# Kernel optimization log

Hardware: AMD Instinct MI355X
Metric: run time of the kernel (lower is better)

## Reference

```python
import jax, jax.numpy as jnp
import numpy as np

EPS = 1e-16


def setup_inputs() -> dict:
    key = jax.random.key(0)
    ks = jax.random.split(key, 7)
    B, N, C = 4096, 2048, 128  # batch of heads, memory rows, memory cols
    k = jax.random.normal(ks[0], (B, C), dtype=jnp.float32)
    beta = jax.random.normal(ks[1], (B, 1), dtype=jnp.float32)
    g = jax.random.normal(ks[2], (B, 1), dtype=jnp.float32)
    s = jax.random.normal(ks[3], (B, 3), dtype=jnp.float32)
    gamma = jax.random.normal(ks[4], (B, 1), dtype=jnp.float32)
    w_prev = jax.random.uniform(ks[5], (B, N), dtype=jnp.float32)
    w_prev = w_prev / jnp.sum(w_prev, axis=1, keepdims=True)  # valid weighting
    M = jax.random.normal(ks[6], (N, C), dtype=jnp.float32)  # memory matrix
    return {"k": k, "beta": beta, "g": g, "s": s, "gamma": gamma,
            "w_prev": w_prev, "M": M}


def reference(k, beta, g, s, gamma, w_prev, M):
    # head activations
    beta = jax.nn.softplus(beta)            # [B,1] key strength > 0
    g = jax.nn.sigmoid(g)                   # [B,1] interpolation gate
    s = jax.nn.softmax(s, axis=-1)          # [B,3] shift distribution
    gamma = 1.0 + jax.nn.softplus(gamma)    # [B,1] sharpening >= 1

    # content addressing: cosine similarity k vs memory rows
    k_norm = jnp.linalg.norm(k, axis=-1, keepdims=True)          # [B,1]
    m_norm = jnp.linalg.norm(M, axis=-1, keepdims=True)          # [N,1]
    sim = jnp.einsum('bc,nc->bn', k, M) / (k_norm * m_norm.T + EPS)  # [B,N]
    w_c = jax.nn.softmax(beta * sim, axis=-1)                    # [B,N]

    # interpolation with previous weighting
    w_g = g * w_c + (1.0 - g) * w_prev                           # [B,N]

    # circular convolution with 3-tap shift kernel (shifts -1, 0, +1)
    w_tilde = (s[:, 0:1] * jnp.roll(w_g, 1, axis=1)
               + s[:, 1:2] * w_g
               + s[:, 2:3] * jnp.roll(w_g, -1, axis=1))          # [B,N]

    # sharpening
    w_sharp = w_tilde ** gamma
    w = w_sharp / (jnp.sum(w_sharp, axis=1, keepdims=True) + EPS)
    return w
```

## Files before the change

### kernel.cpp

```cpp
#include <hip/hip_runtime.h>
#include <math.h>

#define NN 2048
#define CC 128
#define EPSF 1e-16f

typedef __attribute__((ext_vector_type(8))) short bf16x8;
typedef __attribute__((ext_vector_type(4))) float f32x4;

__device__ __forceinline__ float softplusf(float x) {
  return fmaxf(x, 0.0f) + log1pf(__expf(-fabsf(x)));
}
__device__ __forceinline__ float wave_sum(float v) {
#pragma unroll
  for (int o = 32; o; o >>= 1) v += __shfl_xor(v, o, 64);
  return v;
}

union U8 { uint u[4]; bf16x8 v; };

__device__ __forceinline__ void split8(float4 a, float4 b, bf16x8& hi,
                                       bf16x8& lo, float& sq) {
  float f[8] = {a.x, a.y, a.z, a.w, b.x, b.y, b.z, b.w};
  U8 H, L;
#pragma unroll
  for (int i = 0; i < 4; ++i) {
    float f0 = f[2 * i], f1 = f[2 * i + 1];
    sq += f0 * f0;
    sq += f1 * f1;
    uint u0 = __float_as_uint(f0), u1 = __float_as_uint(f1);
    uint m0 = u0 & 0xffff0000u, m1 = u1 & 0xffff0000u;
    float r0 = f0 - __uint_as_float(m0);
    float r1 = f1 - __uint_as_float(m1);
    H.u[i] = (u0 >> 16) | m1;
    L.u[i] = (__float_as_uint(r0) >> 16) | (__float_as_uint(r1) & 0xffff0000u);
  }
  hi = H.v;
  lo = L.v;
}

__global__ __launch_bounds__(256) void ntm_prep_kernel(
    const float* __restrict__ kptr, const float* __restrict__ beta_,
    const float* __restrict__ g_, const float* __restrict__ s_,
    const float* __restrict__ gamma_, const float* __restrict__ M,
    bf16x8* __restrict__ Mhf, bf16x8* __restrict__ Mlf,
    bf16x8* __restrict__ Khf, bf16x8* __restrict__ Klf,
    float* __restrict__ imn, float* __restrict__ zb, float* __restrict__ gvv,
    float* __restrict__ gmv, float* __restrict__ s0a, float* __restrict__ s1a,
    float* __restrict__ s2a) {
  const int bid = blockIdx.x;
  const int t = threadIdx.x;
  if (bid < 96) {
    const int lane = t & 63;
    const int wv = t >> 6;
    const int l15 = lane & 15;
    const int lg = lane >> 4;
    const bool isM = bid < 32;
    const int grp = (isM ? bid : bid - 32) * 4 + wv;
    const int nrow = isM ? ((grp >> 3) * 128 + 8 * l15 + (grp & 7))
                         : (grp * 16 + l15);
    const float* src = (isM ? M : kptr) + nrow * CC + lg * 8;
    bf16x8* dh = (isM ? Mhf : Khf) + (grp * 4) * 64 + lane;
    bf16x8* dl = (isM ? Mlf : Klf) + (grp * 4) * 64 + lane;
    float sq = 0.f;
#pragma unroll
    for (int ks = 0; ks < 4; ++ks) {
      float4 a0 = *(const float4*)(src + ks * 32);
      float4 a1 = *(const float4*)(src + ks * 32 + 4);
      bf16x8 h, l;
      split8(a0, a1, h, l, sq);
      dh[ks * 64] = h;
      dl[ks * 64] = l;
    }
    sq += __shfl_xor(sq, 16, 64);
    sq += __shfl_xor(sq, 32, 64);
    if (lg == 0) {
      if (isM) {
        imn[nrow] = 1.0f / sqrtf(sq);
      } else {
        zb[nrow] = softplusf(beta_[nrow]) / sqrtf(sq);
      }
    }
  } else {
    const int r = (bid - 96) * 256 + t;
    gvv[r] = 1.0f / (1.0f + __expf(-g_[r]));
    gmv[r] = 1.0f + softplusf(gamma_[r]);
    float sh0 = s_[3 * r], sh1 = s_[3 * r + 1], sh2 = s_[3 * r + 2];
    float shm = fmaxf(sh0, fmaxf(sh1, sh2));
    float e0 = __expf(sh0 - shm), e1 = __expf(sh1 - shm), e2 = __expf(sh2 - shm);
    float sden = 1.0f / (e0 + e1 + e2);
    s0a[r] = e0 * sden;
    s1a[r] = e1 * sden;
    s2a[r] = e2 * sden;
  }
}

__global__ __launch_bounds__(1024) void ntm_main_kernel(
    const float* __restrict__ w_prev, const bf16x8* __restrict__ Mhf,
    const bf16x8* __restrict__ Mlf, const bf16x8* __restrict__ Khf,
    const bf16x8* __restrict__ Klf, const float* __restrict__ imn,
    const float* __restrict__ zb, const float* __restrict__ gvv,
    const float* __restrict__ gmv, const float* __restrict__ s0a,
    const float* __restrict__ s1a, const float* __restrict__ s2a,
    float* __restrict__ out) {
  __shared__ float eQ[4][2048];

  const int t = threadIdx.x;
  const int lane = t & 63;
  const int w = __builtin_amdgcn_readfirstlane(t >> 6);
  const int l15 = lane & 15;
  const int lg = lane >> 4;
  const int bg = blockIdx.x;
  const int b0 = bg * 16;

  bf16x8 ah[4], al[4];
#pragma unroll
  for (int ks = 0; ks < 4; ++ks) {
    ah[ks] = Khf[(bg * 4 + ks) * 64 + lane];
    al[ks] = Klf[(bg * 4 + ks) * 64 + lane];
  }

  f32x4 accT[8];
#pragma unroll
  for (int tt = 0; tt < 8; ++tt) accT[tt] = (f32x4){0.f, 0.f, 0.f, 0.f};

#pragma unroll
  for (int ks = 0; ks < 4; ++ks) {
    bf16x8 bh[8], bl[8];
#pragma unroll
    for (int tt = 0; tt < 8; ++tt) {
      const int gM = 8 * w + tt;
      bh[tt] = Mhf[(gM * 4 + ks) * 64 + lane];
      bl[tt] = Mlf[(gM * 4 + ks) * 64 + lane];
    }
#pragma unroll
    for (int tt = 0; tt < 8; ++tt) {
      accT[tt] = __builtin_amdgcn_mfma_f32_16x16x32_bf16(ah[ks], bh[tt], accT[tt], 0, 0, 0);
      accT[tt] = __builtin_amdgcn_mfma_f32_16x16x32_bf16(al[ks], bh[tt], accT[tt], 0, 0, 0);
      accT[tt] = __builtin_amdgcn_mfma_f32_16x16x32_bf16(ah[ks], bl[tt], accT[tt], 0, 0, 0);
    }
  }

  const int ncol0 = 128 * w + 8 * l15;
  const float4 i0 = *(const float4*)&imn[ncol0];
  const float4 i1 = *(const float4*)&imn[ncol0 + 4];
  float imn_t[8] = {i0.x, i0.y, i0.z, i0.w, i1.x, i1.y, i1.z, i1.w};
#pragma unroll
  for (int q = 0; q < 4; ++q) {
    const float zbv = zb[b0 + lg * 4 + q];
#pragma unroll
    for (int tt = 0; tt < 8; ++tt) {
      accT[tt][q] = __expf(accT[tt][q] * imn_t[tt] * zbv);
    }
  }

  float4 v[8];
  const int myq = w & 3;
  const int myr4 = w >> 2;
#pragma unroll
  for (int q = 0; q < 4; ++q) {
    *(float4*)&eQ[lg][ncol0] =
        (float4){accT[0][q], accT[1][q], accT[2][q], accT[3][q]};
    *(float4*)&eQ[lg][ncol0 + 4] =
        (float4){accT[4][q], accT[5][q], accT[6][q], accT[7][q]};
    __syncthreads();
    if (myq == q) {
#pragma unroll
      for (int b = 0; b < 8; ++b)
        v[b] = *(const float4*)&eQ[myr4][256 * b + 4 * lane];
    }
    if (q < 3) __syncthreads();
  }

  const int row = b0 + w;
  const int lanem1 = (lane + 63) & 63;
  const int lanep1 = (lane + 1) & 63;

  float lsum = 0.f;
#pragma unroll
  for (int b = 0; b < 8; ++b)
    lsum += (v[b].x + v[b].y) + (v[b].z + v[b].w);
  const float tot = wave_sum(lsum);

  const float gv = gvv[row];
  const float ge = gv / tot;
  const float om = 1.0f - gv;
  const float sh0 = s0a[row], sh1 = s1a[row], sh2 = s2a[row];
  const float gammav = gmv[row];

  const float4* w_prev4 = (const float4*)w_prev;
  const size_t rf4 = (size_t)row * (NN / 4) + lane;
#pragma unroll
  for (int b = 0; b < 8; ++b) {
    float4 w4 = w_prev4[rf4 + 64 * b];
    v[b].x = ge * v[b].x + om * w4.x;
    v[b].y = ge * v[b].y + om * w4.y;
    v[b].z = ge * v[b].z + om * w4.z;
    v[b].w = ge * v[b].w + om * w4.w;
  }

  float pm[8], np[8];
#pragma unroll
  for (int b = 0; b < 8; ++b) {
    pm[b] = __shfl(v[b].w, lanem1, 64);
    np[b] = __shfl(v[b].x, lanep1, 64);
  }
  float sp = 0.f;
#pragma unroll
  for (int b = 0; b < 8; ++b) {
    const float pv0 = (lane == 0) ? pm[(b + 7) & 7] : pm[b];
    const float nx3 = (lane == 63) ? np[(b + 1) & 7] : np[b];
    const float w0 = v[b].x, w1 = v[b].y, w2 = v[b].z, w3 = v[b].w;
    float t0 = sh0 * pv0 + sh1 * w0 + sh2 * w1;
    float t1 = sh0 * w0 + sh1 * w1 + sh2 * w2;
    float t2 = sh0 * w1 + sh1 * w2 + sh2 * w3;
    float t3 = sh0 * w2 + sh1 * w3 + sh2 * nx3;
    float p0 = __expf(gammav * __logf(t0));
    float p1 = __expf(gammav * __logf(t1));
    float p2 = __expf(gammav * __logf(t2));
    float p3 = __expf(gammav * __logf(t3));
    v[b].x = p0;
    v[b].y = p1;
    v[b].z = p2;
    v[b].w = p3;
    sp += (p0 + p1) + (p2 + p3);
  }
  const float spt = wave_sum(sp);
  const float pinv = 1.0f / (spt + EPSF);

  float4* out4 = (float4*)out;
#pragma unroll
  for (int b = 0; b < 8; ++b) {
    float4 o;
    o.x = v[b].x * pinv;
    o.y = v[b].y * pinv;
    o.z = v[b].z * pinv;
    o.w = v[b].w * pinv;
    out4[rf4 + 64 * b] = o;
  }
}

__global__ __launch_bounds__(1024) void ntm_main_fallback(
    const float* __restrict__ kptr, const float* __restrict__ beta_,
    const float* __restrict__ g_, const float* __restrict__ s_,
    const float* __restrict__ gamma_, const float* __restrict__ w_prev,
    const float* __restrict__ Mptr, float* __restrict__ out) {
  __shared__ float red[16][16];
  __shared__ float edges[16][16][2];
  const int t = threadIdx.x;
  const int lane = t & 63;
  const int w = __builtin_amdgcn_readfirstlane(t >> 6);
  const int l15 = lane & 15;
  const int lg = lane >> 4;
  const int b0 = blockIdx.x * 16;

  const float* kr = kptr + (b0 + l15) * CC + lg * 8;
  bf16x8 ah[4], al[4];
  float ksq = 0.f;
#pragma unroll
  for (int ks = 0; ks < 4; ++ks) {
    float4 a0 = *(const float4*)(kr + ks * 32);
    float4 a1 = *(const float4*)(kr + ks * 32 + 4);
    split8(a0, a1, ah[ks], al[ks], ksq);
  }
  ksq += __shfl_xor(ksq, 16, 64);
  ksq += __shfl_xor(ksq, 32, 64);
  const float ikn_own = 1.0f / sqrtf(ksq);

  f32x4 accT[8];
  float imn[8];
#pragma unroll
  for (int tt = 0; tt < 8; ++tt) {
    const int n0t = 128 * w + 16 * tt;
    const float* mr = Mptr + (size_t)(n0t + l15) * CC + lg * 8;
    f32x4 acc = {0.f, 0.f, 0.f, 0.f};
    float msq = 0.f;
#pragma unroll
    for (int ks = 0; ks < 4; ++ks) {
      float4 m0 = *(const float4*)(mr + ks * 32);
      float4 m1 = *(const float4*)(mr + ks * 32 + 4);
      bf16x8 bh, bl;
      split8(m0, m1, bh, bl, msq);
      acc = __builtin_amdgcn_mfma_f32_16x16x32_bf16(ah[ks], bh, acc, 0, 0, 0);
      acc = __builtin_amdgcn_mfma_f32_16x16x32_bf16(al[ks], bh, acc, 0, 0, 0);
      acc = __builtin_amdgcn_mfma_f32_16x16x32_bf16(ah[ks], bl, acc, 0, 0, 0);
    }
    msq += __shfl_xor(msq, 16, 64);
    msq += __shfl_xor(msq, 32, 64);
    imn[tt] = 1.0f / sqrtf(msq);
    accT[tt] = acc;
  }

#pragma unroll
  for (int q = 0; q < 4; ++q) {
    const int rr = lg * 4 + q;
    const float zb = softplusf(beta_[b0 + rr]) * __shfl(ikn_own, rr, 64);
    float rs = 0.f;
#pragma unroll
    for (int tt = 0; tt < 8; ++tt) {
      float e = __expf(accT[tt][q] * imn[tt] * zb);
      accT[tt][q] = e;
      rs += e;
    }
    rs += __shfl_xor(rs, 1, 64);
    rs += __shfl_xor(rs, 2, 64);
    rs += __shfl_xor(rs, 4, 64);
    rs += __shfl_xor(rs, 8, 64);
    if (l15 == 0) red[rr][w] = rs;
  }
  __syncthreads();

#pragma unroll
  for (int q = 0; q < 4; ++q) {
    const int rr = lg * 4 + q;
    float4 p0 = *(const float4*)&red[rr][0];
    float4 p1 = *(const float4*)&red[rr][4];
    float4 p2 = *(const float4*)&red[rr][8];
    float4 p3 = *(const float4*)&red[rr][12];
    float tot = (p0.x + p0.y + p0.z + p0.w) + (p1.x + p1.y + p1.z + p1.w) +
                (p2.x + p2.y + p2.z + p2.w) + (p3.x + p3.y + p3.z + p3.w);
    const float gv = 1.0f / (1.0f + __expf(-g_[b0 + rr]));
    const float ge = gv / tot;
    const float om = 1.0f - gv;
    const size_t rbase = (size_t)(b0 + rr) * NN + 128 * w + l15;
#pragma unroll
    for (int tt = 0; tt < 8; ++tt) {
      float wpv = w_prev[rbase + 16 * tt];
      accT[tt][q] = ge * accT[tt][q] + om * wpv;
    }
    if (l15 == 0) edges[rr][w][0] = accT[0][q];
    if (l15 == 15) edges[rr][w][1] = accT[7][q];
  }
  __syncthreads();

  const int tm = (lane & 48) | ((lane + 15) & 15);
  const int tp = (lane & 48) | ((lane + 1) & 15);
#pragma unroll
  for (int q = 0; q < 4; ++q) {
    const int rr = lg * 4 + q;
    float sh0 = s_[3 * (b0 + rr)];
    float sh1 = s_[3 * (b0 + rr) + 1];
    float sh2 = s_[3 * (b0 + rr) + 2];
    float shm = fmaxf(sh0, fmaxf(sh1, sh2));
    float e0 = __expf(sh0 - shm), e1 = __expf(sh1 - shm), e2 = __expf(sh2 - shm);
    float sden = 1.0f / (e0 + e1 + e2);
    sh0 = e0 * sden; sh1 = e1 * sden; sh2 = e2 * sden;
    const float gammav = 1.0f + softplusf(gamma_[b0 + rr]);
    const float eL = edges[rr][(w + 15) & 15][1];
    const float eR = edges[rr][(w + 1) & 15][0];
    float sm[8], sp[8];
#pragma unroll
    for (int tt = 0; tt < 8; ++tt) {
      sm[tt] = __shfl(accT[tt][q], tm, 64);
      sp[tt] = __shfl(accT[tt][q], tp, 64);
    }
    float rs = 0.f;
#pragma unroll
    for (int tt = 0; tt < 8; ++tt) {
      float pv = (l15 == 0) ? ((tt == 0) ? eL : sm[tt - 1]) : sm[tt];
      float nx = (l15 == 15) ? ((tt == 7) ? eR : sp[tt + 1]) : sp[tt];
      float wt = sh0 * pv + sh1 * accT[tt][q] + sh2 * nx;
      float p = __expf(gammav * __logf(wt));
      accT[tt][q] = p;
      rs += p;
    }
    rs += __shfl_xor(rs, 1, 64);
    rs += __shfl_xor(rs, 2, 64);
    rs += __shfl_xor(rs, 4, 64);
    rs += __shfl_xor(rs, 8, 64);
    if (l15 == 0) red[rr][w] = rs;
  }
  __syncthreads();

#pragma unroll
  for (int q = 0; q < 4; ++q) {
    const int rr = lg * 4 + q;
    float4 p0 = *(const float4*)&red[rr][0];
    float4 p1 = *(const float4*)&red[rr][4];
    float4 p2 = *(const float4*)&red[rr][8];
    float4 p3 = *(const float4*)&red[rr][12];
    float tot = (p0.x + p0.y + p0.z + p0.w) + (p1.x + p1.y + p1.z + p1.w) +
                (p2.x + p2.y + p2.z + p2.w) + (p3.x + p3.y + p3.z + p3.w);
    const float pinv = 1.0f / (tot + EPSF);
    const size_t rbase = (size_t)(b0 + rr) * NN + 128 * w + l15;
#pragma unroll
    for (int tt = 0; tt < 8; ++tt) {
      out[rbase + 16 * tt] = accT[tt][q] * pinv;
    }
  }
}

extern "C" void kernel_launch(void* const* d_in, const int* in_sizes, int n_in,
                              void* d_out, int out_size, void* d_ws, size_t ws_size,
                              hipStream_t stream) {
  const float* k = (const float*)d_in[0];
  const float* beta = (const float*)d_in[1];
  const float* g = (const float*)d_in[2];
  const float* s = (const float*)d_in[3];
  const float* gamma = (const float*)d_in[4];
  const float* w_prev = (const float*)d_in[5];
  const float* M = (const float*)d_in[6];
  float* out = (float*)d_out;

  char* ws = (char*)d_ws;
  bf16x8* Mhf = (bf16x8*)(ws + 0);
  bf16x8* Mlf = (bf16x8*)(ws + 524288);
  bf16x8* Khf = (bf16x8*)(ws + 1048576);
  bf16x8* Klf = (bf16x8*)(ws + 2097152);
  float* imn = (float*)(ws + 3145728);
  float* zb = imn + 2048;
  float* gvv = zb + 4096;
  float* gmv = gvv + 4096;
  float* s0a = gmv + 4096;
  float* s1a = s0a + 4096;
  float* s2a = s1a + 4096;
  const size_t need = 3145728 + 2048 * 4 + 6 * 4096 * 4;

  if (ws_size >= need) {
    ntm_prep_kernel<<<112, 256, 0, stream>>>(k, beta, g, s, gamma, M, Mhf, Mlf,
                                             Khf, Klf, imn, zb, gvv, gmv, s0a,
                                             s1a, s2a);
    ntm_main_kernel<<<256, 1024, 0, stream>>>(w_prev, Mhf, Mlf, Khf, Klf, imn,
                                              zb, gvv, gmv, s0a, s1a, s2a, out);
  } else {
    ntm_main_fallback<<<256, 1024, 0, stream>>>(k, beta, g, s, gamma, w_prev,
                                                M, out);
  }
}
```

Before: 38.51 us.

## Stream MFMA operands through LDS with async global_load_lds double buffering

Loads the key fragments once into LDS via global_load_lds and streams the memory-matrix fragments per wave through a two-slot LDS ring, using explicit vmcnt/lgkmcnt waits so loads overlap the MFMA chain. The shared buffer grows to 128KB so the full 16x2048 exp tile can be transposed in one pass, replacing four write/sync/read rounds. This lowers register pressure and barrier count, but the large LDS footprint limits occupancy and the manual waitcnt sequencing is fragile.

```diff
diff --git a/kernel.cpp b/kernel.cpp
--- a/kernel.cpp
+++ b/kernel.cpp
@@ -37,6 +37,12 @@
   }
   hi = H.v;
   lo = L.v;
+}
+
+__device__ __forceinline__ void gl2lds16(const void* gsrc, void* ldst) {
+  __builtin_amdgcn_global_load_lds(
+      (const __attribute__((address_space(1))) void*)gsrc,
+      (__attribute__((address_space(3))) void*)ldst, 16, 0, 0);
 }
 
 __global__ __launch_bounds__(256) void ntm_prep_kernel(
@@ -103,7 +109,9 @@
     const float* __restrict__ gmv, const float* __restrict__ s0a,
     const float* __restrict__ s1a, const float* __restrict__ s2a,
     float* __restrict__ out) {
-  __shared__ float eQ[4][2048];
+  __shared__ __align__(16) char smem[131072];
+  char* Areg = smem;
+  float (*eQ)[2048] = (float(*)[2048])smem;
 
   const int t = threadIdx.x;
   const int lane = t & 63;
@@ -113,33 +121,54 @@
   const int bg = blockIdx.x;
   const int b0 = bg * 16;
 
-  bf16x8 ah[4], al[4];
-#pragma unroll
-  for (int ks = 0; ks < 4; ++ks) {
-    ah[ks] = Khf[(bg * 4 + ks) * 64 + lane];
-    al[ks] = Klf[(bg * 4 + ks) * 64 + lane];
-  }
+  if (w == 0) {
+#pragma unroll
+    for (int ks = 0; ks < 4; ++ks) {
+      gl2lds16(&Khf[(bg * 4 + ks) * 64 + lane], Areg + (ks * 2 + 0) * 1024);
+      gl2lds16(&Klf[(bg * 4 + ks) * 64 + lane], Areg + (ks * 2 + 1) * 1024);
+    }
+  }
+  char* myB = smem + 8192 + w * 4096;
+  const int gw = 8 * w;
+#define STAGEB(c)                                                          \
+  {                                                                        \
+    const int ks_ = (c) >> 3, tt_ = (c)&7;                                 \
+    gl2lds16(&Mhf[((gw + tt_) * 4 + ks_) * 64 + lane],                     \
+             myB + ((c)&1) * 2048);                                        \
+    gl2lds16(&Mlf[((gw + tt_) * 4 + ks_) * 64 + lane],                     \
+             myB + ((c)&1) * 2048 + 1024);                                 \
+  }
+  STAGEB(0);
+  STAGEB(1);
+  __syncthreads();
 
   f32x4 accT[8];
 #pragma unroll
   for (int tt = 0; tt < 8; ++tt) accT[tt] = (f32x4){0.f, 0.f, 0.f, 0.f};
 
-#pragma unroll
-  for (int ks = 0; ks < 4; ++ks) {
-    bf16x8 bh[8], bl[8];
-#pragma unroll
-    for (int tt = 0; tt < 8; ++tt) {
-      const int gM = 8 * w + tt;
-      bh[tt] = Mhf[(gM * 4 + ks) * 64 + lane];
-      bl[tt] = Mlf[(gM * 4 + ks) * 64 + lane];
-    }
-#pragma unroll
-    for (int tt = 0; tt < 8; ++tt) {
-      accT[tt] = __builtin_amdgcn_mfma_f32_16x16x32_bf16(ah[ks], bh[tt], accT[tt], 0, 0, 0);
-      accT[tt] = __builtin_amdgcn_mfma_f32_16x16x32_bf16(al[ks], bh[tt], accT[tt], 0, 0, 0);
-      accT[tt] = __builtin_amdgcn_mfma_f32_16x16x32_bf16(ah[ks], bl[tt], accT[tt], 0, 0, 0);
-    }
-  }
+  bf16x8 ah, al;
+#pragma unroll
+  for (int c = 0; c < 32; ++c) {
+    if ((c & 7) == 0) {
+      const int ks_ = c >> 3;
+      ah = *(const bf16x8*)(Areg + (ks_ * 2 + 0) * 1024 + lane * 16);
+      al = *(const bf16x8*)(Areg + (ks_ * 2 + 1) * 1024 + lane * 16);
+    }
+    if (c == 31) {
+      asm volatile("s_waitcnt vmcnt(0)" ::: "memory");
+    } else {
+      asm volatile("s_waitcnt vmcnt(2)" ::: "memory");
+    }
+    bf16x8 bh = *(const bf16x8*)(myB + (c & 1) * 2048 + lane * 16);
+    bf16x8 bl = *(const bf16x8*)(myB + (c & 1) * 2048 + 1024 + lane * 16);
+    asm volatile("s_waitcnt lgkmcnt(0)" ::: "memory");
+    if (c + 2 < 32) STAGEB(c + 2);
+    const int tt = c & 7;
+    accT[tt] = __builtin_amdgcn_mfma_f32_16x16x32_bf16(ah, bh, accT[tt], 0, 0, 0);
+    accT[tt] = __builtin_amdgcn_mfma_f32_16x16x32_bf16(al, bh, accT[tt], 0, 0, 0);
+    accT[tt] = __builtin_amdgcn_mfma_f32_16x16x32_bf16(ah, bl, accT[tt], 0, 0, 0);
+  }
+#undef STAGEB
 
   const int ncol0 = 128 * w + 8 * l15;
   const float4 i0 = *(const float4*)&imn[ncol0];
@@ -154,23 +183,21 @@
     }
   }
 
+  __syncthreads();
+
+#pragma unroll
+  for (int q = 0; q < 4; ++q) {
+    *(float4*)&eQ[lg * 4 + q][ncol0] =
+        (float4){accT[0][q], accT[1][q], accT[2][q], accT[3][q]};
+    *(float4*)&eQ[lg * 4 + q][ncol0 + 4] =
+        (float4){accT[4][q], accT[5][q], accT[6][q], accT[7][q]};
+  }
+  __syncthreads();
+
   float4 v[8];
-  const int myq = w & 3;
-  const int myr4 = w >> 2;
-#pragma unroll
-  for (int q = 0; q < 4; ++q) {
-    *(float4*)&eQ[lg][ncol0] =
-        (float4){accT[0][q], accT[1][q], accT[2][q], accT[3][q]};
-    *(float4*)&eQ[lg][ncol0 + 4] =
-        (float4){accT[4][q], accT[5][q], accT[6][q], accT[7][q]};
-    __syncthreads();
-    if (myq == q) {
-#pragma unroll
-      for (int b = 0; b < 8; ++b)
-        v[b] = *(const float4*)&eQ[myr4][256 * b + 4 * lane];
-    }
-    if (q < 3) __syncthreads();
-  }
+#pragma unroll
+  for (int b = 0; b < 8; ++b)
+    v[b] = *(const float4*)&eQ[w][256 * b + 4 * lane];
 
   const int row = b0 + w;
   const int lanem1 = (lane + 63) & 63;
```

New measurement: 39.25 us. No clear change (+1.9%).
